# Optimization experiments

Hardware: AMD Instinct MI355X
Metric: run time of the kernel (lower is better)

## Reference

```python
import jax, jax.numpy as jnp
import numpy as np

N = 100000
E = 1600000
IN_C = 128
HID = 64


def setup_inputs() -> dict:
    key = jax.random.key(0)
    ks = jax.random.split(key, 8)
    x = jax.random.normal(ks[0], (N, IN_C), dtype=jnp.float32)
    edge_index = jax.random.randint(ks[1], (2, E), 0, N, dtype=jnp.int64)
    # Glorot-ish init for faithfulness; exact init values don't matter for correctness baseline
    W1 = jax.random.normal(ks[2], (IN_C, HID), dtype=jnp.float32) / np.sqrt(IN_C)
    b1 = jnp.zeros((HID,), dtype=jnp.float32)
    W2 = jax.random.normal(ks[3], (HID, HID), dtype=jnp.float32) / np.sqrt(HID)
    b2 = jnp.zeros((HID,), dtype=jnp.float32)
    Wc = jax.random.normal(ks[4], (HID, 1), dtype=jnp.float32) / np.sqrt(HID)
    bc = jnp.zeros((1,), dtype=jnp.float32)
    return {"x": x, "edge_index": edge_index, "W1": W1, "b1": b1,
            "W2": W2, "b2": b2, "Wc": Wc, "bc": bc}


def _gcn_conv(x, W, b, src, dst, norm, n_nodes):
    # PyG GCNConv: h = x @ W; out[dst] += norm * h[src]; out += b
    h = x @ W                                  # [N, out_c]
    msg = h[src] * norm[:, None]               # [E+N, out_c] gather + scale
    out = jax.ops.segment_sum(msg, dst, num_segments=n_nodes)  # scatter-add
    return out + b


def reference(x, edge_index, W1, b1, W2, b2, Wc, bc):
    n = x.shape[0]
    loop = jnp.arange(n, dtype=edge_index.dtype)
    src = jnp.concatenate([edge_index[0], loop])   # add self-loops (PyG default)
    dst = jnp.concatenate([edge_index[1], loop])
    # symmetric normalization: deg over destination (col) including self-loops
    deg = jax.ops.segment_sum(jnp.ones_like(dst, dtype=x.dtype), dst, num_segments=n)
    dinv = jnp.where(deg > 0, jax.lax.rsqrt(deg), 0.0)
    norm = dinv[src] * dinv[dst]                   # [E+N]

    h = jax.nn.relu(_gcn_conv(x, W1, b1, src, dst, norm, n))
    h = jax.nn.relu(_gcn_conv(h, W2, b2, src, dst, norm, n))
    logits = (h @ Wc + bc)[:, 0]                   # squeeze(-1)
    return logits
```

## Files before the change

kernel.cpp:

```cpp
#include <hip/hip_runtime.h>
#include <hip/hip_fp16.h>


#define IN_C 128
#define HID  64
#define CAP  64
#define NBUCKET 256
#define BCHUNK  391
#define BUCKET_CAP 8192
#define EPB 2048

typedef __attribute__((ext_vector_type(4))) _Float16 half4;

__global__ void k_zero_i32(int* __restrict__ p, int n) {
    int i = blockIdx.x * blockDim.x + threadIdx.x;
    if (i < n) p[i] = 0;
}

__global__ void k_partition(const int* __restrict__ ei, int* __restrict__ cursor,
                            int2* __restrict__ ebuf, int E) {
    __shared__ int2 stage[EPB];
    __shared__ unsigned char sbkt[EPB];
    __shared__ int cnt[NBUCKET];
    __shared__ int pfx[NBUCKET];
    __shared__ int bstart[NBUCKET];
    __shared__ int gbase[NBUCKET];

    int t = threadIdx.x;
    int e0 = blockIdx.x * EPB;
    cnt[t] = 0;
    __syncthreads();

    int  myb[EPB / 256];
    int2 myv[EPB / 256];
    #pragma unroll
    for (int i = 0; i < EPB / 256; ++i) {
        int e = e0 + i * 256 + t;
        int b = -1; int2 v = make_int2(0, 0);
        if (e < E) {
            v.x = ei[e];
            v.y = ei[E + e];
            b = v.y / BCHUNK;
            atomicAdd(&cnt[b], 1);
        }
        myb[i] = b; myv[i] = v;
    }
    __syncthreads();

    int c = cnt[t];
    pfx[t] = c;
    __syncthreads();
    #pragma unroll
    for (int off = 1; off < NBUCKET; off <<= 1) {
        int u = (t >= off) ? pfx[t - off] : 0;
        __syncthreads();
        pfx[t] += u;
        __syncthreads();
    }
    bstart[t] = pfx[t] - c;
    gbase[t]  = atomicAdd(&cursor[t], c);
    cnt[t] = 0;
    __syncthreads();

    #pragma unroll
    for (int i = 0; i < EPB / 256; ++i) {
        int b = myb[i];
        if (b >= 0) {
            int pos = bstart[b] + atomicAdd(&cnt[b], 1);
            stage[pos] = myv[i];
            sbkt[pos]  = (unsigned char)b;
        }
    }
    __syncthreads();

    int total = pfx[NBUCKET - 1];
    for (int i = t; i < total; i += 256) {
        int b = sbkt[i];
        int off = gbase[b] + (i - bstart[b]);
        if (off < BUCKET_CAP)
            ebuf[(long)b * BUCKET_CAP + off] = stage[i];
    }
}

__global__ void k_fill_bucket(const int2* __restrict__ ebuf, const int* __restrict__ cursor,
                              int* __restrict__ deg, float* __restrict__ dinv,
                              int* __restrict__ pairs, int n) {
    __shared__ int lcur[BCHUNK];
    int t = threadIdx.x;
    int b = blockIdx.x;
    int lo = b * BCHUNK;
    int hi = min(n, lo + BCHUNK);
    for (int i = t; i < BCHUNK; i += 256) lcur[i] = 0;
    __syncthreads();

    int cnt = min(cursor[b], BUCKET_CAP);
    const int2* p = ebuf + (long)b * BUCKET_CAP;
    for (int i = t; i < cnt; i += 256) {
        int2 v = p[i];
        int pos = atomicAdd(&lcur[v.y - lo], 1);
        if (pos < CAP) pairs[(long)v.y * CAP + pos] = v.x;
    }
    __syncthreads();
    for (int i = lo + t; i < hi; i += 256) {
        int d = lcur[i - lo];
        deg[i]  = d;
        dinv[i] = rsqrtf((float)(d + 1));
    }
}

template <int K>
__global__ void k_gemm64_h(const float* __restrict__ X, const float* __restrict__ W,
                           const float* __restrict__ dinv, _Float16* __restrict__ H, int n) {
    __shared__ float Ws[K * 64];
    for (int i = threadIdx.x * 4; i < K * 64; i += 256 * 4)
        *(float4*)&Ws[i] = *(const float4*)&W[i];
    __syncthreads();

    int tx = threadIdx.x & 15;
    int ty = threadIdx.x >> 4;
    int row0 = blockIdx.x * 64 + ty * 4;
    if (row0 >= n) return;
    int c4 = tx * 4;

    const float* xr[4];
    #pragma unroll
    for (int r = 0; r < 4; ++r) xr[r] = X + (long)min(row0 + r, n - 1) * K;

    float4 acc[4];
    #pragma unroll
    for (int r = 0; r < 4; ++r) acc[r] = make_float4(0.f, 0.f, 0.f, 0.f);

    #pragma unroll 4
    for (int k = 0; k < K; k += 4) {
        float4 xv[4];
        #pragma unroll
        for (int r = 0; r < 4; ++r) xv[r] = *(const float4*)&xr[r][k];
        #pragma unroll
        for (int kk = 0; kk < 4; ++kk) {
            float4 w = *(const float4*)&Ws[(k + kk) * 64 + c4];
            #pragma unroll
            for (int r = 0; r < 4; ++r) {
                float xs = (kk == 0) ? xv[r].x : (kk == 1) ? xv[r].y
                         : (kk == 2) ? xv[r].z : xv[r].w;
                acc[r].x = fmaf(xs, w.x, acc[r].x);
                acc[r].y = fmaf(xs, w.y, acc[r].y);
                acc[r].z = fmaf(xs, w.z, acc[r].z);
                acc[r].w = fmaf(xs, w.w, acc[r].w);
            }
        }
    }

    #pragma unroll
    for (int r = 0; r < 4; ++r)
        if (row0 + r < n) {
            float dv = dinv[row0 + r];
            half4 h;
            h.x = (_Float16)(dv * acc[r].x); h.y = (_Float16)(dv * acc[r].y);
            h.z = (_Float16)(dv * acc[r].z); h.w = (_Float16)(dv * acc[r].w);
            *(half4*)&H[(long)(row0 + r) * 64 + c4] = h;
        }
}

__device__ __forceinline__ float4 gather_sum(const _Float16* __restrict__ H,
                                             int4 q, int cnt, int gb, int c4,
                                             float4 acc) {
    int jj = 0;
    for (; jj + 8 <= cnt; jj += 8) {
        int sl = gb + (jj >> 2);
        int a0 = __shfl(q.x, sl, 64),     a1 = __shfl(q.y, sl, 64);
        int a2 = __shfl(q.z, sl, 64),     a3 = __shfl(q.w, sl, 64);
        int b0 = __shfl(q.x, sl + 1, 64), b1 = __shfl(q.y, sl + 1, 64);
        int b2 = __shfl(q.z, sl + 1, 64), b3 = __shfl(q.w, sl + 1, 64);
        half4 v0 = *(const half4*)&H[(long)a0 * 64 + c4];
        half4 v1 = *(const half4*)&H[(long)a1 * 64 + c4];
        half4 v2 = *(const half4*)&H[(long)a2 * 64 + c4];
        half4 v3 = *(const half4*)&H[(long)a3 * 64 + c4];
        half4 v4 = *(const half4*)&H[(long)b0 * 64 + c4];
        half4 v5 = *(const half4*)&H[(long)b1 * 64 + c4];
        half4 v6 = *(const half4*)&H[(long)b2 * 64 + c4];
        half4 v7 = *(const half4*)&H[(long)b3 * 64 + c4];
        acc.x += (float)v0.x + (float)v1.x + (float)v2.x + (float)v3.x
               + (float)v4.x + (float)v5.x + (float)v6.x + (float)v7.x;
        acc.y += (float)v0.y + (float)v1.y + (float)v2.y + (float)v3.y
               + (float)v4.y + (float)v5.y + (float)v6.y + (float)v7.y;
        acc.z += (float)v0.z + (float)v1.z + (float)v2.z + (float)v3.z
               + (float)v4.z + (float)v5.z + (float)v6.z + (float)v7.z;
        acc.w += (float)v0.w + (float)v1.w + (float)v2.w + (float)v3.w
               + (float)v4.w + (float)v5.w + (float)v6.w + (float)v7.w;
    }
    if (jj < cnt) {
        int sl = gb + (jj >> 2);
        int s[8];
        s[0] = __shfl(q.x, sl, 64);     s[1] = __shfl(q.y, sl, 64);
        s[2] = __shfl(q.z, sl, 64);     s[3] = __shfl(q.w, sl, 64);
        s[4] = __shfl(q.x, sl + 1, 64); s[5] = __shfl(q.y, sl + 1, 64);
        s[6] = __shfl(q.z, sl + 1, 64); s[7] = __shfl(q.w, sl + 1, 64);
        #pragma unroll
        for (int u = 0; u < 8; ++u) {
            bool ok = (jj + u) < cnt;
            int sc = ok ? s[u] : 0;
            half4 v = *(const half4*)&H[(long)sc * 64 + c4];
            float w = ok ? 1.f : 0.f;
            acc.x = fmaf((float)v.x, w, acc.x);
            acc.y = fmaf((float)v.y, w, acc.y);
            acc.z = fmaf((float)v.z, w, acc.z);
            acc.w = fmaf((float)v.w, w, acc.w);
        }
    }
    return acc;
}

__global__ void k_gather_fuse(const _Float16* __restrict__ H, const int* __restrict__ pairs,
                              const int* __restrict__ deg, const float* __restrict__ dinv,
                              const float* __restrict__ b1, const float* __restrict__ W2,
                              _Float16* __restrict__ OUT, int n) {
    __shared__ float Ws[64 * 64];
    for (int i = threadIdx.x * 4; i < 64 * 64; i += 256 * 4)
        *(float4*)&Ws[i] = *(const float4*)&W2[i];
    __syncthreads();

    int t = blockIdx.x * blockDim.x + threadIdx.x;
    int node = t >> 4;
    int l16  = threadIdx.x & 15;
    int gb   = (threadIdx.x & 63) & ~15;
    if (node >= n) return;
    int c4 = l16 * 4;

    float di = dinv[node];
    int cnt  = min(deg[node], CAP);
    int4 q = *(const int4*)&pairs[(long)node * CAP + l16 * 4];

    half4 h0 = *(const half4*)&H[(long)node * 64 + c4];
    float4 acc = make_float4((float)h0.x, (float)h0.y, (float)h0.z, (float)h0.w);
    acc = gather_sum(H, q, cnt, gb, c4, acc);

    float4 bb = *(const float4*)&b1[c4];
    float4 r = make_float4(fmaxf(fmaf(di, acc.x, bb.x), 0.f),
                           fmaxf(fmaf(di, acc.y, bb.y), 0.f),
                           fmaxf(fmaf(di, acc.z, bb.z), 0.f),
                           fmaxf(fmaf(di, acc.w, bb.w), 0.f));
    float4 o = make_float4(0.f, 0.f, 0.f, 0.f);
    #pragma unroll
    for (int j = 0; j < 16; ++j) {
        float4 bv;
        bv.x = __shfl(r.x, j, 16); bv.y = __shfl(r.y, j, 16);
        bv.z = __shfl(r.z, j, 16); bv.w = __shfl(r.w, j, 16);
        float4 w0 = *(const float4*)&Ws[(j * 4 + 0) * 64 + c4];
        float4 w1 = *(const float4*)&Ws[(j * 4 + 1) * 64 + c4];
        float4 w2 = *(const float4*)&Ws[(j * 4 + 2) * 64 + c4];
        float4 w3 = *(const float4*)&Ws[(j * 4 + 3) * 64 + c4];
        o.x = fmaf(bv.x, w0.x, o.x); o.y = fmaf(bv.x, w0.y, o.y);
        o.z = fmaf(bv.x, w0.z, o.z); o.w = fmaf(bv.x, w0.w, o.w);
        o.x = fmaf(bv.y, w1.x, o.x); o.y = fmaf(bv.y, w1.y, o.y);
        o.z = fmaf(bv.y, w1.z, o.z); o.w = fmaf(bv.y, w1.w, o.w);
        o.x = fmaf(bv.z, w2.x, o.x); o.y = fmaf(bv.z, w2.y, o.y);
        o.z = fmaf(bv.z, w2.z, o.z); o.w = fmaf(bv.z, w2.w, o.w);
        o.x = fmaf(bv.w, w3.x, o.x); o.y = fmaf(bv.w, w3.y, o.y);
        o.z = fmaf(bv.w, w3.z, o.z); o.w = fmaf(bv.w, w3.w, o.w);
    }
    half4 ho;
    ho.x = (_Float16)(di * o.x); ho.y = (_Float16)(di * o.y);
    ho.z = (_Float16)(di * o.z); ho.w = (_Float16)(di * o.w);
    *(half4*)&OUT[(long)node * 64 + c4] = ho;
}

__global__ void k_gather_head(const _Float16* __restrict__ H, const int* __restrict__ pairs,
                              const int* __restrict__ deg, const float* __restrict__ dinv,
                              const float* __restrict__ b2, const float* __restrict__ Wc,
                              const float* __restrict__ bc, float* __restrict__ OUT, int n) {
    int t = blockIdx.x * blockDim.x + threadIdx.x;
    int node = t >> 4;
    int l16  = threadIdx.x & 15;
    int gb   = (threadIdx.x & 63) & ~15;
    if (node >= n) return;
    int c4 = l16 * 4;

    float di = dinv[node];
    int cnt  = min(deg[node], CAP);
    int4 q = *(const int4*)&pairs[(long)node * CAP + l16 * 4];

    half4 h0 = *(const half4*)&H[(long)node * 64 + c4];
    float4 acc = make_float4((float)h0.x, (float)h0.y, (float)h0.z, (float)h0.w);
    acc = gather_sum(H, q, cnt, gb, c4, acc);

    float4 bb = *(const float4*)&b2[c4];
    float4 wc = *(const float4*)&Wc[c4];
    float v = fmaxf(fmaf(di, acc.x, bb.x), 0.f) * wc.x +
              fmaxf(fmaf(di, acc.y, bb.y), 0.f) * wc.y +
              fmaxf(fmaf(di, acc.z, bb.z), 0.f) * wc.z +
              fmaxf(fmaf(di, acc.w, bb.w), 0.f) * wc.w;
    v += __shfl_down(v, 8, 16);
    v += __shfl_down(v, 4, 16);
    v += __shfl_down(v, 2, 16);
    v += __shfl_down(v, 1, 16);
    if (l16 == 0) OUT[node] = v + bc[0];
}

extern "C" void kernel_launch(void* const* d_in, const int* in_sizes, int n_in,
                              void* d_out, int out_size, void* d_ws, size_t ws_size,
                              hipStream_t stream) {
    const float* x  = (const float*)d_in[0];
    const int*   ei = (const int*)d_in[1];
    const float* W1 = (const float*)d_in[2];
    const float* b1 = (const float*)d_in[3];
    const float* W2 = (const float*)d_in[4];
    const float* b2 = (const float*)d_in[5];
    const float* Wc = (const float*)d_in[6];
    const float* bc = (const float*)d_in[7];
    float* out = (float*)d_out;

    const int n = in_sizes[0] / IN_C;
    const int E = in_sizes[1] / 2;

    char* w = (char*)d_ws;
    auto alloc = [&](size_t bytes) { char* r = w; w += (bytes + 255) & ~(size_t)255; return r; };
    int*      deg    = (int*)alloc((size_t)n * 4);
    float*    dinv   = (float*)alloc((size_t)n * 4);
    int*      pairs  = (int*)alloc((size_t)n * CAP * 4);
    _Float16* A16    = (_Float16*)alloc((size_t)n * HID * 2);
    _Float16* B16    = (_Float16*)alloc((size_t)n * HID * 2);
    int*      cursor = (int*)alloc(NBUCKET * 4);
    int2*     ebuf   = (int2*)alloc((size_t)NBUCKET * BUCKET_CAP * 8);

    const int BS = 256;
    dim3 blk(BS);
    auto grid_items = [&](long items) { return dim3((unsigned)((items + BS - 1) / BS)); };

    k_zero_i32<<<dim3(1), blk, 0, stream>>>(cursor, NBUCKET);
    k_partition<<<dim3((unsigned)((E + EPB - 1) / EPB)), blk, 0, stream>>>(ei, cursor, ebuf, E);
    k_fill_bucket<<<dim3(NBUCKET), blk, 0, stream>>>(ebuf, cursor, deg, dinv, pairs, n);

    k_gemm64_h<IN_C><<<dim3((n + 63) / 64), blk, 0, stream>>>(x, W1, dinv, A16, n);

    k_gather_fuse<<<grid_items((long)n * 16), blk, 0, stream>>>(
        A16, pairs, deg, dinv, b1, W2, B16, n);

    k_gather_head<<<grid_items((long)n * 16), blk, 0, stream>>>(
        B16, pairs, deg, dinv, b2, Wc, bc, out, n);
}
```

Measured before the change: 246.9 us.

## Replace first-layer FMA GEMM with fp16 MFMA persistent-wave kernel

The first X@W1 projection now runs on matrix cores via 16x16x32 fp16 MFMA instructions instead of scalar FMAs with W staged in shared memory. W1 fragments are held in registers per wave, and a fixed grid of 1024 blocks loops over 16-row tiles. Inputs are rounded to fp16 before multiplication, which loses some precision. Output stores become scattered 2-byte writes instead of half4 vectors. The GEMM reads 51MB of X, so it is likely bandwidth-bound and the compute savings may be limited.

```diff
diff --git a/kernel.cpp b/kernel.cpp
--- a/kernel.cpp
+++ b/kernel.cpp
@@ -11,6 +11,8 @@
 #define EPB 2048
 
 typedef __attribute__((ext_vector_type(4))) _Float16 half4;
+typedef __attribute__((ext_vector_type(8))) _Float16 half8;
+typedef __attribute__((ext_vector_type(4))) float f32x4;
 
 __global__ void k_zero_i32(int* __restrict__ p, int n) {
     int i = blockIdx.x * blockDim.x + threadIdx.x;
@@ -108,57 +110,67 @@
     }
 }
 
-template <int K>
-__global__ void k_gemm64_h(const float* __restrict__ X, const float* __restrict__ W,
-                           const float* __restrict__ dinv, _Float16* __restrict__ H, int n) {
-    __shared__ float Ws[K * 64];
-    for (int i = threadIdx.x * 4; i < K * 64; i += 256 * 4)
-        *(float4*)&Ws[i] = *(const float4*)&W[i];
-    __syncthreads();
-
-    int tx = threadIdx.x & 15;
-    int ty = threadIdx.x >> 4;
-    int row0 = blockIdx.x * 64 + ty * 4;
-    if (row0 >= n) return;
-    int c4 = tx * 4;
-
-    const float* xr[4];
-    #pragma unroll
-    for (int r = 0; r < 4; ++r) xr[r] = X + (long)min(row0 + r, n - 1) * K;
-
-    float4 acc[4];
-    #pragma unroll
-    for (int r = 0; r < 4; ++r) acc[r] = make_float4(0.f, 0.f, 0.f, 0.f);
-
-    #pragma unroll 4
-    for (int k = 0; k < K; k += 4) {
-        float4 xv[4];
-        #pragma unroll
-        for (int r = 0; r < 4; ++r) xv[r] = *(const float4*)&xr[r][k];
-        #pragma unroll
-        for (int kk = 0; kk < 4; ++kk) {
-            float4 w = *(const float4*)&Ws[(k + kk) * 64 + c4];
+__launch_bounds__(256)
+__global__ void k_gemm1_mfma(const float* __restrict__ X, const float* __restrict__ W,
+                             const float* __restrict__ dinv, _Float16* __restrict__ H,
+                             int n) {
+    int lane = threadIdx.x & 63;
+    int m    = lane & 15;
+    int quad = lane >> 4;
+    int wid  = blockIdx.x * (blockDim.x >> 6) + (threadIdx.x >> 6);
+    int nwav = gridDim.x * (blockDim.x >> 6);
+
+    half8 wf[4][4];
+    #pragma unroll
+    for (int ks = 0; ks < 4; ++ks)
+        #pragma unroll
+        for (int ct = 0; ct < 4; ++ct)
             #pragma unroll
-            for (int r = 0; r < 4; ++r) {
-                float xs = (kk == 0) ? xv[r].x : (kk == 1) ? xv[r].y
-                         : (kk == 2) ? xv[r].z : xv[r].w;
-                acc[r].x = fmaf(xs, w.x, acc[r].x);
-                acc[r].y = fmaf(xs, w.y, acc[r].y);
-                acc[r].z = fmaf(xs, w.z, acc[r].z);
-                acc[r].w = fmaf(xs, w.w, acc[r].w);
+            for (int j = 0; j < 8; ++j)
+                wf[ct][ks][j] = (_Float16)W[(ks * 32 + quad * 8 + j) * 64 + ct * 16 + m];
+
+    int ntile = (n + 15) >> 4;
+    for (int tile = wid; tile < ntile; tile += nwav) {
+        int row0 = tile << 4;
+        const float* xr = X + (long)min(row0 + m, n - 1) * IN_C;
+
+        float4 xa[4], xb[4];
+        #pragma unroll
+        for (int ks = 0; ks < 4; ++ks) {
+            xa[ks] = *(const float4*)&xr[ks * 32 + quad * 8];
+            xb[ks] = *(const float4*)&xr[ks * 32 + quad * 8 + 4];
+        }
+        half8 af[4];
+        #pragma unroll
+        for (int ks = 0; ks < 4; ++ks) {
+            af[ks][0] = (_Float16)xa[ks].x; af[ks][1] = (_Float16)xa[ks].y;
+            af[ks][2] = (_Float16)xa[ks].z; af[ks][3] = (_Float16)xa[ks].w;
+            af[ks][4] = (_Float16)xb[ks].x; af[ks][5] = (_Float16)xb[ks].y;
+            af[ks][6] = (_Float16)xb[ks].z; af[ks][7] = (_Float16)xb[ks].w;
+        }
+
+        f32x4 acc0 = {0.f, 0.f, 0.f, 0.f}, acc1 = acc0, acc2 = acc0, acc3 = acc0;
+        #pragma unroll
+        for (int ks = 0; ks < 4; ++ks) {
+            acc0 = __builtin_amdgcn_mfma_f32_16x16x32_f16(af[ks], wf[0][ks], acc0, 0, 0, 0);
+            acc1 = __builtin_amdgcn_mfma_f32_16x16x32_f16(af[ks], wf[1][ks], acc1, 0, 0, 0);
+            acc2 = __builtin_amdgcn_mfma_f32_16x16x32_f16(af[ks], wf[2][ks], acc2, 0, 0, 0);
+            acc3 = __builtin_amdgcn_mfma_f32_16x16x32_f16(af[ks], wf[3][ks], acc3, 0, 0, 0);
+        }
+
+        #pragma unroll
+        for (int r = 0; r < 4; ++r) {
+            int row = row0 + quad * 4 + r;
+            if (row < n) {
+                float dv = dinv[row];
+                _Float16* hp = H + (long)row * 64 + m;
+                hp[0]  = (_Float16)(dv * acc0[r]);
+                hp[16] = (_Float16)(dv * acc1[r]);
+                hp[32] = (_Float16)(dv * acc2[r]);
+                hp[48] = (_Float16)(dv * acc3[r]);
             }
         }
     }
-
-    #pragma unroll
-    for (int r = 0; r < 4; ++r)
-        if (row0 + r < n) {
-            float dv = dinv[row0 + r];
-            half4 h;
-            h.x = (_Float16)(dv * acc[r].x); h.y = (_Float16)(dv * acc[r].y);
-            h.z = (_Float16)(dv * acc[r].z); h.w = (_Float16)(dv * acc[r].w);
-            *(half4*)&H[(long)(row0 + r) * 64 + c4] = h;
-        }
 }
 
 __device__ __forceinline__ float4 gather_sum(const _Float16* __restrict__ H,
@@ -330,7 +342,7 @@
     k_partition<<<dim3((unsigned)((E + EPB - 1) / EPB)), blk, 0, stream>>>(ei, cursor, ebuf, E);
     k_fill_bucket<<<dim3(NBUCKET), blk, 0, stream>>>(ebuf, cursor, deg, dinv, pairs, n);
 
-    k_gemm64_h<IN_C><<<dim3((n + 63) / 64), blk, 0, stream>>>(x, W1, dinv, A16, n);
+    k_gemm1_mfma<<<dim3(1024), blk, 0, stream>>>(x, W1, dinv, A16, n);
 
     k_gather_fuse<<<grid_items((long)n * 16), blk, 0, stream>>>(
         A16, pairs, deg, dinv, b1, W2, B16, n);
```

Result: faster. 227.9 us (-7.7%).
